# Kernel optimization log

Hardware: AMD Instinct MI355X
Metric: run time of the kernel (lower is better)

## Reference

```python
import jax, jax.numpy as jnp
import numpy as np

N_NODES = 200000
N_PATCHES = 256
TIMESTEPS = 12
NHID = 16
HORIZON = 12
IN_DIM = NHID * TIMESTEPS + TIMESTEPS  # 204


def setup_inputs() -> dict:
    key = jax.random.key(0)
    ks = jax.random.split(key, 6)
    mixer_x = jax.random.normal(ks[0], (1, TIMESTEPS, N_PATCHES, NHID), dtype=jnp.float32)
    features = jax.random.normal(ks[1], (N_NODES, TIMESTEPS), dtype=jnp.float32)
    W1 = jax.random.normal(ks[2], (IN_DIM, IN_DIM), dtype=jnp.float32) * (1.0 / np.sqrt(IN_DIM))
    b1 = jnp.zeros((IN_DIM,), dtype=jnp.float32)
    W2 = jax.random.normal(ks[3], (IN_DIM, HORIZON), dtype=jnp.float32) * (1.0 / np.sqrt(IN_DIM))
    b2 = jnp.zeros((HORIZON,), dtype=jnp.float32)
    node_patch = jax.random.randint(ks[4], (N_NODES,), 0, N_PATCHES, dtype=jnp.int32)
    return {"mixer_x": mixer_x, "features": features, "W1": W1, "b1": b1,
            "W2": W2, "b2": b2, "node_patch": node_patch}


def reference(mixer_x, features, W1, b1, W2, b2, node_patch):
    # mixer_x: (b, t, p, f) -> per-patch flattened features 'b p (t f)'
    b, t, p, f = mixer_x.shape
    patch_feat = jnp.transpose(mixer_x, (0, 2, 1, 3)).reshape(b, p, t * f)
    # per-node gather of its patch's features: (b, N, t*f)
    g = jnp.take(patch_feat, node_patch, axis=1)
    # node features broadcast over batch: (b, N, t)
    node_x = jnp.broadcast_to(features[None], (b,) + features.shape)
    x = jnp.concatenate([g, node_x], axis=-1)  # (b, N, in_dim)
    h = jax.nn.relu(jnp.einsum('bni,ij->bnj', x, W1) + b1)
    out = jnp.einsum('bnh,ho->bno', h, W2) + b2  # (1, N, horizon)
    return out
```

## Files before the change

### kernel.cpp

```cpp
#include <hip/hip_runtime.h>
#include <hip/hip_bf16.h>

#define N_NODES   200000
#define N_PATCHES 256
#define TSTEPS    12
#define NHID      16
#define HORIZON   12
#define GDIM      192
#define IN_DIM    204
#define PH_STRIDE 206
#define PH_STRIDE_DW 103
#define NCHUNKS   6250
#define K2_THREADS 512
#define TOTAL_WAVES 2048
#define TBL_U4    6592

typedef __attribute__((ext_vector_type(8)))  short        bf16x8;
typedef __attribute__((ext_vector_type(16))) float        f32x16;
typedef __attribute__((ext_vector_type(4)))  unsigned int u32x4;

__device__ __forceinline__ unsigned int pk2(float lo, float hi) {
    unsigned short l = __builtin_bit_cast(unsigned short, __float2bfloat16(lo));
    unsigned short h = __builtin_bit_cast(unsigned short, __float2bfloat16(hi));
    return ((unsigned int)h << 16) | (unsigned int)l;
}

__device__ __forceinline__ bf16x8 frag_of(unsigned int a, unsigned int b,
                                          unsigned int c, unsigned int d) {
    u32x4 u; u[0] = a; u[1] = b; u[2] = c; u[3] = d;
    return __builtin_bit_cast(bf16x8, u);
}

__device__ __forceinline__ float bf16bits_lo(unsigned int w) {
    return __builtin_bit_cast(float, w << 16);
}
__device__ __forceinline__ float bf16bits_hi(unsigned int w) {
    return __builtin_bit_cast(float, w & 0xffff0000u);
}

__device__ __forceinline__ void gload_lds16(const uint4* g, uint4* l) {
    __builtin_amdgcn_global_load_lds(
        (const __attribute__((address_space(1))) unsigned int*)g,
        (__attribute__((address_space(3))) unsigned int*)l,
        16, 0, 0);
}

__device__ __forceinline__ float ldW1f(const float* __restrict__ W1, int k, int j) {
    const bool ok = (k < TSTEPS) && (j < IN_DIM);
    const int  idx = ok ? ((GDIM + k) * IN_DIM + j) : 0;
    const float v = W1[idx];
    return ok ? v : 0.0f;
}
__device__ __forceinline__ float ldW2t(const float* __restrict__ W2, int j, int o) {
    const bool ok = (j < IN_DIM) && (o < HORIZON);
    const int  idx = ok ? (j * HORIZON + o) : 0;
    const float v = W2[idx];
    return ok ? v : 0.0f;
}

__global__ __launch_bounds__(1024) void precompute(
    const float* __restrict__ mixer_x,
    const float* __restrict__ W1,
    const float* __restrict__ b1,
    const float* __restrict__ W2,
    unsigned short* __restrict__ patch_hb,
    u32x4* __restrict__ wfrag)
{
    const int blk = blockIdx.x;
    const int tid = threadIdx.x;

    if (blk == N_PATCHES) {
        const int lane = tid & 63;
        const int g    = tid >> 6;
        const int jl   = lane & 31;
        const int kb   = 4 * (lane >> 5);
        for (int f = g; f < 20; f += 16) {
            u32x4 u;
            if (f < 7) {
                const int j = f * 32 + jl;
                u[0] = pk2(ldW1f(W1, kb + 0,  j), ldW1f(W1, kb + 1,  j));
                u[1] = pk2(ldW1f(W1, kb + 2,  j), ldW1f(W1, kb + 3,  j));
                u[2] = pk2(ldW1f(W1, kb + 8,  j), ldW1f(W1, kb + 9,  j));
                u[3] = pk2(ldW1f(W1, kb + 10, j), ldW1f(W1, kb + 11, j));
            } else {
                const int j0 = (f - 7) * 16 + kb;
                u[0] = pk2(ldW2t(W2, j0 + 0,  jl), ldW2t(W2, j0 + 1,  jl));
                u[1] = pk2(ldW2t(W2, j0 + 2,  jl), ldW2t(W2, j0 + 3,  jl));
                u[2] = pk2(ldW2t(W2, j0 + 8,  jl), ldW2t(W2, j0 + 9,  jl));
                u[3] = pk2(ldW2t(W2, j0 + 10, jl), ldW2t(W2, j0 + 11, jl));
            }
            wfrag[f * 64 + lane] = u;
        }
        return;
    }

    __shared__ float xs[GDIM];
    __shared__ float partial[3 * IN_DIM];
    const int p = blk;
    const int j = tid & 255;
    const int q = tid >> 8;

    if (tid < GDIM) {
        const int t = tid >> 4, f = tid & 15;
        xs[tid] = mixer_x[(t * N_PATCHES + p) * NHID + f];
    }
    __syncthreads();

    float acc = 0.0f;
    if (j < IN_DIM) {
        acc = (q == 0) ? b1[j] : 0.0f;
        const int ibase = q * 48;
#pragma unroll 16
        for (int i = 0; i < 48; ++i)
            acc = fmaf(xs[ibase + i], W1[(ibase + i) * IN_DIM + j], acc);
        if (q > 0) partial[(q - 1) * IN_DIM + j] = acc;
    }
    __syncthreads();
    if (q == 0 && j < IN_DIM) {
        const float v = acc + partial[j] + partial[IN_DIM + j] + partial[2 * IN_DIM + j];
        patch_hb[p * PH_STRIDE + j] =
            __builtin_bit_cast(unsigned short, __float2bfloat16(v));
    }
}

__global__ __launch_bounds__(K2_THREADS) void node_mlp_mfma(
    const float* __restrict__ features,
    const int*   __restrict__ node_patch,
    const unsigned short* __restrict__ patch_hb,
    const u32x4* __restrict__ wfrag,
    const float* __restrict__ b2,
    float* __restrict__ out)
{
    __shared__ unsigned short smem[N_PATCHES * PH_STRIDE];

    const int tid  = threadIdx.x;
    const int lane = tid & 63;
    const int wid  = tid >> 6;
    const int jl   = lane & 31;
    const int hi   = lane >> 5;

    int c = blockIdx.x * 8 + wid;
    float4 fa, fb, fc; int p;
    {
        const float4* fp = (const float4*)(features + (c * 32 + jl) * TSTEPS);
        fa = fp[0]; fb = fp[1]; fc = fp[2];
        p  = node_patch[c * 32 + jl];
    }

    bf16x8 A1f[7], A2f[13];
#pragma unroll
    for (int f = 0; f < 7; ++f)
        A1f[f] = __builtin_bit_cast(bf16x8, wfrag[f * 64 + lane]);
#pragma unroll
    for (int f = 0; f < 13; ++f)
        A2f[f] = __builtin_bit_cast(bf16x8, wfrag[(7 + f) * 64 + lane]);

    const float4 b2A = *(const float4*)(b2 + 4 * hi);
    const float4 b2B = *(const float4*)(b2 + 8);

    {
        const uint4* src = (const uint4*)patch_hb;
        uint4* dst = (uint4*)smem;
#pragma unroll
        for (int k = 0; k < 13; ++k) {
            const int i = tid + k * K2_THREADS;
            if (i < TBL_U4) gload_lds16(src + i, dst + i);
        }
    }
    __syncthreads();

    while (true) {
        const int  cn    = c + TOTAL_WAVES;
        const bool haveN = (cn < NCHUNKS);
        float4 fa2, fb2, fc2; int p2 = 0;
        if (haveN) {
            const float4* fq = (const float4*)(features + (cn * 32 + jl) * TSTEPS);
            fa2 = fq[0]; fb2 = fq[1]; fc2 = fq[2];
            p2  = node_patch[cn * 32 + jl];
        }

        const bf16x8 B1 = frag_of(hi ? pk2(fb.x, fb.y) : pk2(fa.x, fa.y),
                                  hi ? pk2(fb.z, fb.w) : pk2(fa.z, fa.w),
                                  hi ? 0u              : pk2(fc.x, fc.y),
                                  hi ? 0u              : pk2(fc.z, fc.w));

        const unsigned int* dwrow =
            (const unsigned int*)smem + p * PH_STRIDE_DW;

        f32x16 oE, oO;
#pragma unroll
        for (int e = 0; e < 16; ++e) { oE[e] = 0.0f; oO[e] = 0.0f; }

        unsigned int nx[8];
#pragma unroll
        for (int G = 0; G < 4; ++G) {
            const int di = 4 * G + 2 * hi;
            nx[2 * G]     = dwrow[di];
            nx[2 * G + 1] = dwrow[di + 1];
        }

#pragma unroll
        for (int t = 0; t < 7; ++t) {
            unsigned int cu[8];
#pragma unroll
            for (int g = 0; g < 8; ++g) cu[g] = nx[g];

            if (t < 6) {
#pragma unroll
                for (int G = 0; G < 4; ++G) {
                    const int e  = (t + 1) * 32 + 8 * G + 4 * hi;
                    const bool ok = (e <= 200);
                    const int di = ok ? (e >> 1) : 0;
                    nx[2 * G]     = dwrow[di];
                    nx[2 * G + 1] = dwrow[di + 1];
                }
            }

            f32x16 acc;
#pragma unroll
            for (int G = 0; G < 4; ++G) {
                const bool ok = (t * 32 + 8 * G + 4 * hi) <= 200;
                acc[4 * G + 0] = ok ? bf16bits_lo(cu[2 * G])     : 0.0f;
                acc[4 * G + 1] = ok ? bf16bits_hi(cu[2 * G])     : 0.0f;
                acc[4 * G + 2] = ok ? bf16bits_lo(cu[2 * G + 1]) : 0.0f;
                acc[4 * G + 3] = ok ? bf16bits_hi(cu[2 * G + 1]) : 0.0f;
            }

            acc = __builtin_amdgcn_mfma_f32_32x32x16_bf16(A1f[t], B1, acc, 0, 0, 0);

            const bf16x8 ba = frag_of(
                pk2(fmaxf(acc[0], 0.f), fmaxf(acc[1], 0.f)),
                pk2(fmaxf(acc[2], 0.f), fmaxf(acc[3], 0.f)),
                pk2(fmaxf(acc[4], 0.f), fmaxf(acc[5], 0.f)),
                pk2(fmaxf(acc[6], 0.f), fmaxf(acc[7], 0.f)));
            oE = __builtin_amdgcn_mfma_f32_32x32x16_bf16(A2f[2 * t], ba, oE, 0, 0, 0);

            if (t < 6) {
                const bf16x8 bb = frag_of(
                    pk2(fmaxf(acc[8],  0.f), fmaxf(acc[9],  0.f)),
                    pk2(fmaxf(acc[10], 0.f), fmaxf(acc[11], 0.f)),
                    pk2(fmaxf(acc[12], 0.f), fmaxf(acc[13], 0.f)),
                    pk2(fmaxf(acc[14], 0.f), fmaxf(acc[15], 0.f)));
                oO = __builtin_amdgcn_mfma_f32_32x32x16_bf16(A2f[2 * t + 1], bb, oO, 0, 0, 0);
            }
        }

        {
            const int node = c * 32 + jl;
            float* orow = out + node * HORIZON;
            const float s0 = oE[0] + oO[0], s1 = oE[1] + oO[1];
            const float s2 = oE[2] + oO[2], s3 = oE[3] + oO[3];
            if (hi == 0) {
                const float s4 = oE[4] + oO[4], s5 = oE[5] + oO[5];
                const float s6 = oE[6] + oO[6], s7 = oE[7] + oO[7];
                *(float4*)(orow + 0) = make_float4(s0 + b2A.x, s1 + b2A.y,
                                                   s2 + b2A.z, s3 + b2A.w);
                *(float4*)(orow + 8) = make_float4(s4 + b2B.x, s5 + b2B.y,
                                                   s6 + b2B.z, s7 + b2B.w);
            } else {
                *(float4*)(orow + 4) = make_float4(s0 + b2A.x, s1 + b2A.y,
                                                   s2 + b2A.z, s3 + b2A.w);
            }
        }

        if (!haveN) break;
        fa = fa2; fb = fb2; fc = fc2; p = p2; c = cn;
    }
}

extern "C" void kernel_launch(void* const* d_in, const int* in_sizes, int n_in,
                              void* d_out, int out_size, void* d_ws, size_t ws_size,
                              hipStream_t stream) {
    const float* mixer_x    = (const float*)d_in[0];
    const float* features   = (const float*)d_in[1];
    const float* W1         = (const float*)d_in[2];
    const float* b1         = (const float*)d_in[3];
    const float* W2         = (const float*)d_in[4];
    const float* b2         = (const float*)d_in[5];
    const int*   node_patch = (const int*)d_in[6];
    float* out = (float*)d_out;

    unsigned short* patch_hb = (unsigned short*)d_ws;
    u32x4*          wfrag    = (u32x4*)((char*)d_ws + 105472);

    precompute<<<257, 1024, 0, stream>>>(mixer_x, W1, b1, W2, patch_hb, wfrag);

    node_mlp_mfma<<<256, K2_THREADS, 0, stream>>>(features, node_patch,
                                                  patch_hb, wfrag, b2, out);
}
```

Before: 25.06 us.

## Fuse patch precompute into node kernel, computing patch table per block via MFMA

Removes the separate precompute launch and the global workspace round-trip. Each of the 256 blocks now builds the bf16 weight fragments and recomputes the full 256x204 patch-hidden table into LDS, using bf16 MFMA over mixer_x and W1. This saves a kernel launch and the inter-kernel dependency. In exchange every block repeats the whole patch GEMM, and its inputs are rounded to bf16 where the old path accumulated in fp32.

```diff
diff --git a/kernel.cpp b/kernel.cpp
--- a/kernel.cpp
+++ b/kernel.cpp
@@ -11,9 +11,8 @@
 #define PH_STRIDE 206
 #define PH_STRIDE_DW 103
 #define NCHUNKS   6250
-#define K2_THREADS 512
+#define THREADS   512
 #define TOTAL_WAVES 2048
-#define TBL_U4    6592
 
 typedef __attribute__((ext_vector_type(8)))  short        bf16x8;
 typedef __attribute__((ext_vector_type(16))) float        f32x16;
@@ -36,13 +35,6 @@
 }
 __device__ __forceinline__ float bf16bits_hi(unsigned int w) {
     return __builtin_bit_cast(float, w & 0xffff0000u);
-}
-
-__device__ __forceinline__ void gload_lds16(const uint4* g, uint4* l) {
-    __builtin_amdgcn_global_load_lds(
-        (const __attribute__((address_space(1))) unsigned int*)g,
-        (__attribute__((address_space(3))) unsigned int*)l,
-        16, 0, 0);
 }
 
 __device__ __forceinline__ float ldW1f(const float* __restrict__ W1, int k, int j) {
@@ -58,116 +50,108 @@
     return ok ? v : 0.0f;
 }
 
-__global__ __launch_bounds__(1024) void precompute(
+__global__ __launch_bounds__(THREADS) void fused_mlp(
     const float* __restrict__ mixer_x,
+    const float* __restrict__ features,
     const float* __restrict__ W1,
     const float* __restrict__ b1,
     const float* __restrict__ W2,
-    unsigned short* __restrict__ patch_hb,
-    u32x4* __restrict__ wfrag)
-{
-    const int blk = blockIdx.x;
-    const int tid = threadIdx.x;
-
-    if (blk == N_PATCHES) {
-        const int lane = tid & 63;
-        const int g    = tid >> 6;
-        const int jl   = lane & 31;
-        const int kb   = 4 * (lane >> 5);
-        for (int f = g; f < 20; f += 16) {
-            u32x4 u;
-            if (f < 7) {
-                const int j = f * 32 + jl;
-                u[0] = pk2(ldW1f(W1, kb + 0,  j), ldW1f(W1, kb + 1,  j));
-                u[1] = pk2(ldW1f(W1, kb + 2,  j), ldW1f(W1, kb + 3,  j));
-                u[2] = pk2(ldW1f(W1, kb + 8,  j), ldW1f(W1, kb + 9,  j));
-                u[3] = pk2(ldW1f(W1, kb + 10, j), ldW1f(W1, kb + 11, j));
-            } else {
-                const int j0 = (f - 7) * 16 + kb;
-                u[0] = pk2(ldW2t(W2, j0 + 0,  jl), ldW2t(W2, j0 + 1,  jl));
-                u[1] = pk2(ldW2t(W2, j0 + 2,  jl), ldW2t(W2, j0 + 3,  jl));
-                u[2] = pk2(ldW2t(W2, j0 + 8,  jl), ldW2t(W2, j0 + 9,  jl));
-                u[3] = pk2(ldW2t(W2, j0 + 10, jl), ldW2t(W2, j0 + 11, jl));
-            }
-            wfrag[f * 64 + lane] = u;
-        }
-        return;
-    }
-
-    __shared__ float xs[GDIM];
-    __shared__ float partial[3 * IN_DIM];
-    const int p = blk;
-    const int j = tid & 255;
-    const int q = tid >> 8;
-
-    if (tid < GDIM) {
-        const int t = tid >> 4, f = tid & 15;
-        xs[tid] = mixer_x[(t * N_PATCHES + p) * NHID + f];
-    }
-    __syncthreads();
-
-    float acc = 0.0f;
-    if (j < IN_DIM) {
-        acc = (q == 0) ? b1[j] : 0.0f;
-        const int ibase = q * 48;
-#pragma unroll 16
-        for (int i = 0; i < 48; ++i)
-            acc = fmaf(xs[ibase + i], W1[(ibase + i) * IN_DIM + j], acc);
-        if (q > 0) partial[(q - 1) * IN_DIM + j] = acc;
-    }
-    __syncthreads();
-    if (q == 0 && j < IN_DIM) {
-        const float v = acc + partial[j] + partial[IN_DIM + j] + partial[2 * IN_DIM + j];
-        patch_hb[p * PH_STRIDE + j] =
-            __builtin_bit_cast(unsigned short, __float2bfloat16(v));
-    }
-}
-
-__global__ __launch_bounds__(K2_THREADS) void node_mlp_mfma(
-    const float* __restrict__ features,
+    const float* __restrict__ b2,
     const int*   __restrict__ node_patch,
-    const unsigned short* __restrict__ patch_hb,
-    const u32x4* __restrict__ wfrag,
-    const float* __restrict__ b2,
     float* __restrict__ out)
 {
-    __shared__ unsigned short smem[N_PATCHES * PH_STRIDE];
+    __shared__ unsigned short ph[N_PATCHES * PH_STRIDE];
+    __shared__ u32x4 wfl[20 * 64];
 
     const int tid  = threadIdx.x;
     const int lane = tid & 63;
     const int wid  = tid >> 6;
     const int jl   = lane & 31;
     const int hi   = lane >> 5;
+    const int kb   = 4 * hi;
 
     int c = blockIdx.x * 8 + wid;
     float4 fa, fb, fc; int p;
     {
-        const float4* fp = (const float4*)(features + (c * 32 + jl) * TSTEPS);
-        fa = fp[0]; fb = fp[1]; fc = fp[2];
+        const float4* fp0 = (const float4*)(features + (c * 32 + jl) * TSTEPS);
+        fa = fp0[0]; fb = fp0[1]; fc = fp0[2];
         p  = node_patch[c * 32 + jl];
     }
-
-    bf16x8 A1f[7], A2f[13];
-#pragma unroll
-    for (int f = 0; f < 7; ++f)
-        A1f[f] = __builtin_bit_cast(bf16x8, wfrag[f * 64 + lane]);
-#pragma unroll
-    for (int f = 0; f < 13; ++f)
-        A2f[f] = __builtin_bit_cast(bf16x8, wfrag[(7 + f) * 64 + lane]);
-
     const float4 b2A = *(const float4*)(b2 + 4 * hi);
     const float4 b2B = *(const float4*)(b2 + 8);
 
-    {
-        const uint4* src = (const uint4*)patch_hb;
-        uint4* dst = (uint4*)smem;
-#pragma unroll
-        for (int k = 0; k < 13; ++k) {
-            const int i = tid + k * K2_THREADS;
-            if (i < TBL_U4) gload_lds16(src + i, dst + i);
-        }
-    }
+    for (int f = wid; f < 20; f += 8) {
+        u32x4 u;
+        if (f < 7) {
+            const int j = f * 32 + jl;
+            u[0] = pk2(ldW1f(W1, kb + 0,  j), ldW1f(W1, kb + 1,  j));
+            u[1] = pk2(ldW1f(W1, kb + 2,  j), ldW1f(W1, kb + 3,  j));
+            u[2] = pk2(ldW1f(W1, kb + 8,  j), ldW1f(W1, kb + 9,  j));
+            u[3] = pk2(ldW1f(W1, kb + 10, j), ldW1f(W1, kb + 11, j));
+        } else {
+            const int j0 = (f - 7) * 16 + kb;
+            u[0] = pk2(ldW2t(W2, j0 + 0,  jl), ldW2t(W2, j0 + 1,  jl));
+            u[1] = pk2(ldW2t(W2, j0 + 2,  jl), ldW2t(W2, j0 + 3,  jl));
+            u[2] = pk2(ldW2t(W2, j0 + 8,  jl), ldW2t(W2, j0 + 9,  jl));
+            u[3] = pk2(ldW2t(W2, j0 + 10, jl), ldW2t(W2, j0 + 11, jl));
+        }
+        wfl[f * 64 + lane] = u;
+    }
+
+    if (wid < 7) {
+        const int j0 = wid * 32;
+        const int jc = (j0 + jl < IN_DIM) ? (j0 + jl) : (IN_DIM - 1);
+
+        bf16x8 Bf[12];
+#pragma unroll
+        for (int kt = 0; kt < 12; ++kt) {
+            const int r = kt * 16 + kb;
+            Bf[kt] = frag_of(
+                pk2(W1[(r + 0)  * IN_DIM + jc], W1[(r + 1)  * IN_DIM + jc]),
+                pk2(W1[(r + 2)  * IN_DIM + jc], W1[(r + 3)  * IN_DIM + jc]),
+                pk2(W1[(r + 8)  * IN_DIM + jc], W1[(r + 9)  * IN_DIM + jc]),
+                pk2(W1[(r + 10) * IN_DIM + jc], W1[(r + 11) * IN_DIM + jc]));
+        }
+        const float bini = b1[jc];
+        const bool  jok  = (j0 + jl < IN_DIM);
+
+        for (int pt = 0; pt < 8; ++pt) {
+            const float* xb = mixer_x + (pt * 32 + jl) * NHID;
+
+            f32x16 acc;
+#pragma unroll
+            for (int e = 0; e < 16; ++e) acc[e] = bini;
+
+#pragma unroll
+            for (int kt = 0; kt < 12; ++kt) {
+                const float* xk = xb + kt * (N_PATCHES * NHID);
+                const float4 xa = *(const float4*)(xk + kb);
+                const float4 xc = *(const float4*)(xk + 8 + kb);
+                const bf16x8 Af = frag_of(pk2(xa.x, xa.y), pk2(xa.z, xa.w),
+                                          pk2(xc.x, xc.y), pk2(xc.z, xc.w));
+                acc = __builtin_amdgcn_mfma_f32_32x32x16_bf16(Af, Bf[kt], acc, 0, 0, 0);
+            }
+
+            if (jok) {
+#pragma unroll
+                for (int e = 0; e < 16; ++e) {
+                    const int prow = pt * 32 + (e & 3) + 8 * (e >> 2) + 4 * hi;
+                    ph[prow * PH_STRIDE + j0 + jl] =
+                        __builtin_bit_cast(unsigned short, __float2bfloat16(acc[e]));
+                }
+            }
+        }
+    }
+
     __syncthreads();
+
+    bf16x8 A1f[7], A2f[13];
+#pragma unroll
+    for (int f = 0; f < 7; ++f)
+        A1f[f] = __builtin_bit_cast(bf16x8, wfl[f * 64 + lane]);
+#pragma unroll
+    for (int f = 0; f < 13; ++f)
+        A2f[f] = __builtin_bit_cast(bf16x8, wfl[(7 + f) * 64 + lane]);
 
     while (true) {
         const int  cn    = c + TOTAL_WAVES;
@@ -184,8 +168,7 @@
                                   hi ? 0u              : pk2(fc.x, fc.y),
                                   hi ? 0u              : pk2(fc.z, fc.w));
 
-        const unsigned int* dwrow =
-            (const unsigned int*)smem + p * PH_STRIDE_DW;
+        const unsigned int* dwrow = (const unsigned int*)ph + p * PH_STRIDE_DW;
 
         f32x16 oE, oO;
 #pragma unroll
@@ -280,11 +263,6 @@
     const int*   node_patch = (const int*)d_in[6];
     float* out = (float*)d_out;
 
-    unsigned short* patch_hb = (unsigned short*)d_ws;
-    u32x4*          wfrag    = (u32x4*)((char*)d_ws + 105472);
-
-    precompute<<<257, 1024, 0, stream>>>(mixer_x, W1, b1, W2, patch_hb, wfrag);
-
-    node_mlp_mfma<<<256, K2_THREADS, 0, stream>>>(features, node_patch,
-                                                  patch_hb, wfrag, b2, out);
-}
+    fused_mlp<<<256, THREADS, 0, stream>>>(mixer_x, features, W1, b1, W2, b2,
+                                           node_patch, out);
+}
```

After: 39.17 us. +56.3%, slower.

## Process two node chunks per wave iteration to interleave independent MFMA chains

Applied to the files above, without the earlier changes.

Each wave now handles a pair of 32-node chunks per loop iteration, running two independent MFMA dependency chains side by side to hide MFMA latency. The LDS patch rows are loaded directly into the accumulator init per tile instead of being prefetched one tile ahead. The cross-iteration prefetch of the next chunk's features is removed, and loads happen after the stores. This raises register pressure and changes the work distribution to 3125 pairs over 2048 waves, which can worsen tail imbalance.

```diff
diff --git a/kernel.cpp b/kernel.cpp
--- a/kernel.cpp
+++ b/kernel.cpp
@@ -10,7 +10,7 @@
 #define IN_DIM    204
 #define PH_STRIDE 206
 #define PH_STRIDE_DW 103
-#define NCHUNKS   6250
+#define NPAIRS    3125
 #define K2_THREADS 512
 #define TOTAL_WAVES 2048
 #define TBL_U4    6592
@@ -56,6 +56,22 @@
     const int  idx = ok ? (j * HORIZON + o) : 0;
     const float v = W2[idx];
     return ok ? v : 0.0f;
+}
+
+__device__ __forceinline__ void cinit_tile(const unsigned int* __restrict__ dwrow,
+                                           int t, int hi, f32x16& acc) {
+#pragma unroll
+    for (int G = 0; G < 4; ++G) {
+        const int e  = t * 32 + 8 * G + 4 * hi;
+        const bool ok = (e <= 200);
+        const int di = ok ? (e >> 1) : 0;
+        const unsigned int r0 = dwrow[di];
+        const unsigned int r1 = dwrow[di + 1];
+        acc[4 * G + 0] = ok ? bf16bits_lo(r0) : 0.0f;
+        acc[4 * G + 1] = ok ? bf16bits_hi(r0) : 0.0f;
+        acc[4 * G + 2] = ok ? bf16bits_lo(r1) : 0.0f;
+        acc[4 * G + 3] = ok ? bf16bits_hi(r1) : 0.0f;
+    }
 }
 
 __global__ __launch_bounds__(1024) void precompute(
@@ -139,12 +155,17 @@
     const int jl   = lane & 31;
     const int hi   = lane >> 5;
 
-    int c = blockIdx.x * 8 + wid;
-    float4 fa, fb, fc; int p;
+    int pr = blockIdx.x * 8 + wid;
+    float4 faA, fbA, fcA, faB, fbB, fcB; int pA, pB;
     {
-        const float4* fp = (const float4*)(features + (c * 32 + jl) * TSTEPS);
-        fa = fp[0]; fb = fp[1]; fc = fp[2];
-        p  = node_patch[c * 32 + jl];
+        const int nA = pr * 64 + jl;
+        const int nB = nA + 32;
+        const float4* fpA = (const float4*)(features + nA * TSTEPS);
+        const float4* fpB = (const float4*)(features + nB * TSTEPS);
+        faA = fpA[0]; fbA = fpA[1]; fcA = fpA[2];
+        faB = fpB[0]; fbB = fpB[1]; fcB = fpB[2];
+        pA  = node_patch[nA];
+        pB  = node_patch[nB];
     }
 
     bf16x8 A1f[7], A2f[13];
@@ -170,89 +191,70 @@
     __syncthreads();
 
     while (true) {
-        const int  cn    = c + TOTAL_WAVES;
-        const bool haveN = (cn < NCHUNKS);
-        float4 fa2, fb2, fc2; int p2 = 0;
-        if (haveN) {
-            const float4* fq = (const float4*)(features + (cn * 32 + jl) * TSTEPS);
-            fa2 = fq[0]; fb2 = fq[1]; fc2 = fq[2];
-            p2  = node_patch[cn * 32 + jl];
-        }
-
-        const bf16x8 B1 = frag_of(hi ? pk2(fb.x, fb.y) : pk2(fa.x, fa.y),
-                                  hi ? pk2(fb.z, fb.w) : pk2(fa.z, fa.w),
-                                  hi ? 0u              : pk2(fc.x, fc.y),
-                                  hi ? 0u              : pk2(fc.z, fc.w));
-
-        const unsigned int* dwrow =
-            (const unsigned int*)smem + p * PH_STRIDE_DW;
-
-        f32x16 oE, oO;
-#pragma unroll
-        for (int e = 0; e < 16; ++e) { oE[e] = 0.0f; oO[e] = 0.0f; }
-
-        unsigned int nx[8];
-#pragma unroll
-        for (int G = 0; G < 4; ++G) {
-            const int di = 4 * G + 2 * hi;
-            nx[2 * G]     = dwrow[di];
-            nx[2 * G + 1] = dwrow[di + 1];
+        const bf16x8 B1A = frag_of(hi ? pk2(fbA.x, fbA.y) : pk2(faA.x, faA.y),
+                                   hi ? pk2(fbA.z, fbA.w) : pk2(faA.z, faA.w),
+                                   hi ? 0u                : pk2(fcA.x, fcA.y),
+                                   hi ? 0u                : pk2(fcA.z, fcA.w));
+        const bf16x8 B1B = frag_of(hi ? pk2(fbB.x, fbB.y) : pk2(faB.x, faB.y),
+                                   hi ? pk2(fbB.z, fbB.w) : pk2(faB.z, faB.w),
+                                   hi ? 0u                : pk2(fcB.x, fcB.y),
+                                   hi ? 0u                : pk2(fcB.z, fcB.w));
+
+        const unsigned int* rowA = (const unsigned int*)smem + pA * PH_STRIDE_DW;
+        const unsigned int* rowB = (const unsigned int*)smem + pB * PH_STRIDE_DW;
+
+        f32x16 oEA, oOA, oEB, oOB;
+#pragma unroll
+        for (int e = 0; e < 16; ++e) {
+            oEA[e] = 0.0f; oOA[e] = 0.0f; oEB[e] = 0.0f; oOB[e] = 0.0f;
         }
 
 #pragma unroll
         for (int t = 0; t < 7; ++t) {
-            unsigned int cu[8];
-#pragma unroll
-            for (int g = 0; g < 8; ++g) cu[g] = nx[g];
+            f32x16 accA, accB;
+            cinit_tile(rowA, t, hi, accA);
+            cinit_tile(rowB, t, hi, accB);
+
+            accA = __builtin_amdgcn_mfma_f32_32x32x16_bf16(A1f[t], B1A, accA, 0, 0, 0);
+            accB = __builtin_amdgcn_mfma_f32_32x32x16_bf16(A1f[t], B1B, accB, 0, 0, 0);
+
+            const bf16x8 baA = frag_of(
+                pk2(fmaxf(accA[0], 0.f), fmaxf(accA[1], 0.f)),
+                pk2(fmaxf(accA[2], 0.f), fmaxf(accA[3], 0.f)),
+                pk2(fmaxf(accA[4], 0.f), fmaxf(accA[5], 0.f)),
+                pk2(fmaxf(accA[6], 0.f), fmaxf(accA[7], 0.f)));
+            const bf16x8 baB = frag_of(
+                pk2(fmaxf(accB[0], 0.f), fmaxf(accB[1], 0.f)),
+                pk2(fmaxf(accB[2], 0.f), fmaxf(accB[3], 0.f)),
+                pk2(fmaxf(accB[4], 0.f), fmaxf(accB[5], 0.f)),
+                pk2(fmaxf(accB[6], 0.f), fmaxf(accB[7], 0.f)));
+            oEA = __builtin_amdgcn_mfma_f32_32x32x16_bf16(A2f[2 * t], baA, oEA, 0, 0, 0);
+            oEB = __builtin_amdgcn_mfma_f32_32x32x16_bf16(A2f[2 * t], baB, oEB, 0, 0, 0);
 
             if (t < 6) {
-#pragma unroll
-                for (int G = 0; G < 4; ++G) {
-                    const int e  = (t + 1) * 32 + 8 * G + 4 * hi;
-                    const bool ok = (e <= 200);
-                    const int di = ok ? (e >> 1) : 0;
-                    nx[2 * G]     = dwrow[di];
-                    nx[2 * G + 1] = dwrow[di + 1];
-                }
+                const bf16x8 bbA = frag_of(
+                    pk2(fmaxf(accA[8],  0.f), fmaxf(accA[9],  0.f)),
+                    pk2(fmaxf(accA[10], 0.f), fmaxf(accA[11], 0.f)),
+                    pk2(fmaxf(accA[12], 0.f), fmaxf(accA[13], 0.f)),
+                    pk2(fmaxf(accA[14], 0.f), fmaxf(accA[15], 0.f)));
+                const bf16x8 bbB = frag_of(
+                    pk2(fmaxf(accB[8],  0.f), fmaxf(accB[9],  0.f)),
+                    pk2(fmaxf(accB[10], 0.f), fmaxf(accB[11], 0.f)),
+                    pk2(fmaxf(accB[12], 0.f), fmaxf(accB[13], 0.f)),
+                    pk2(fmaxf(accB[14], 0.f), fmaxf(accB[15], 0.f)));
+                oOA = __builtin_amdgcn_mfma_f32_32x32x16_bf16(A2f[2 * t + 1], bbA, oOA, 0, 0, 0);
+                oOB = __builtin_amdgcn_mfma_f32_32x32x16_bf16(A2f[2 * t + 1], bbB, oOB, 0, 0, 0);
             }
-
-            f32x16 acc;
-#pragma unroll
-            for (int G = 0; G < 4; ++G) {
-                const bool ok = (t * 32 + 8 * G + 4 * hi) <= 200;
-                acc[4 * G + 0] = ok ? bf16bits_lo(cu[2 * G])     : 0.0f;
-                acc[4 * G + 1] = ok ? bf16bits_hi(cu[2 * G])     : 0.0f;
-                acc[4 * G + 2] = ok ? bf16bits_lo(cu[2 * G + 1]) : 0.0f;
-                acc[4 * G + 3] = ok ? bf16bits_hi(cu[2 * G + 1]) : 0.0f;
-            }
-
-            acc = __builtin_amdgcn_mfma_f32_32x32x16_bf16(A1f[t], B1, acc, 0, 0, 0);
-
-            const bf16x8 ba = frag_of(
-                pk2(fmaxf(acc[0], 0.f), fmaxf(acc[1], 0.f)),
-                pk2(fmaxf(acc[2], 0.f), fmaxf(acc[3], 0.f)),
-                pk2(fmaxf(acc[4], 0.f), fmaxf(acc[5], 0.f)),
-                pk2(fmaxf(acc[6], 0.f), fmaxf(acc[7], 0.f)));
-            oE = __builtin_amdgcn_mfma_f32_32x32x16_bf16(A2f[2 * t], ba, oE, 0, 0, 0);
-
-            if (t < 6) {
-                const bf16x8 bb = frag_of(
-                    pk2(fmaxf(acc[8],  0.f), fmaxf(acc[9],  0.f)),
-                    pk2(fmaxf(acc[10], 0.f), fmaxf(acc[11], 0.f)),
-                    pk2(fmaxf(acc[12], 0.f), fmaxf(acc[13], 0.f)),
-                    pk2(fmaxf(acc[14], 0.f), fmaxf(acc[15], 0.f)));
-                oO = __builtin_amdgcn_mfma_f32_32x32x16_bf16(A2f[2 * t + 1], bb, oO, 0, 0, 0);
-            }
         }
 
         {
-            const int node = c * 32 + jl;
-            float* orow = out + node * HORIZON;
-            const float s0 = oE[0] + oO[0], s1 = oE[1] + oO[1];
-            const float s2 = oE[2] + oO[2], s3 = oE[3] + oO[3];
+            const int nA = pr * 64 + jl;
+            float* orow = out + nA * HORIZON;
+            const float s0 = oEA[0] + oOA[0], s1 = oEA[1] + oOA[1];
+            const float s2 = oEA[2] + oOA[2], s3 = oEA[3] + oOA[3];
             if (hi == 0) {
-                const float s4 = oE[4] + oO[4], s5 = oE[5] + oO[5];
-                const float s6 = oE[6] + oO[6], s7 = oE[7] + oO[7];
+                const float s4 = oEA[4] + oOA[4], s5 = oEA[5] + oOA[5];
+                const float s6 = oEA[6] + oOA[6], s7 = oEA[7] + oOA[7];
                 *(float4*)(orow + 0) = make_float4(s0 + b2A.x, s1 + b2A.y,
                                                    s2 + b2A.z, s3 + b2A.w);
                 *(float4*)(orow + 8) = make_float4(s4 + b2B.x, s5 + b2B.y,
@@ -262,9 +264,35 @@
                                                    s2 + b2A.z, s3 + b2A.w);
             }
         }
-
-        if (!haveN) break;
-        fa = fa2; fb = fb2; fc = fc2; p = p2; c = cn;
+        {
+            const int nB = pr * 64 + 32 + jl;
+            float* orow = out + nB * HORIZON;
+            const float s0 = oEB[0] + oOB[0], s1 = oEB[1] + oOB[1];
+            const float s2 = oEB[2] + oOB[2], s3 = oEB[3] + oOB[3];
+            if (hi == 0) {
+                const float s4 = oEB[4] + oOB[4], s5 = oEB[5] + oOB[5];
+                const float s6 = oEB[6] + oOB[6], s7 = oEB[7] + oOB[7];
+                *(float4*)(orow + 0) = make_float4(s0 + b2A.x, s1 + b2A.y,
+                                                   s2 + b2A.z, s3 + b2A.w);
+                *(float4*)(orow + 8) = make_float4(s4 + b2B.x, s5 + b2B.y,
+                                                   s6 + b2B.z, s7 + b2B.w);
+            } else {
+                *(float4*)(orow + 4) = make_float4(s0 + b2A.x, s1 + b2A.y,
+                                                   s2 + b2A.z, s3 + b2A.w);
+            }
+        }
+
+        pr += TOTAL_WAVES;
+        if (pr >= NPAIRS) break;
+
+        const int nA = pr * 64 + jl;
+        const int nB = nA + 32;
+        const float4* fpA = (const float4*)(features + nA * TSTEPS);
+        const float4* fpB = (const float4*)(features + nB * TSTEPS);
+        faA = fpA[0]; fbA = fpA[1]; fcA = fpA[2];
+        faB = fpB[0]; fbB = fpB[1]; fcB = fpB[2];
+        pA  = node_patch[nA];
+        pB  = node_patch[nB];
     }
 }
 
```

Result: slower. 26.14 us (+4.3%).
